# Kernel optimization log

Hardware: AMD Instinct MI355X
Metric: run time of the kernel (lower is better)

## Reference

```python
import jax, jax.numpy as jnp
import numpy as np

NEG_BIG = -1e30  # stand-in for -inf in the log-space eps state


def wkv_scan(w, u, k, v, alpha0, beta0, eps0):
    """Numerically-stable RWKV WKV recurrence.

    w: exp(time_decay) (D,), u: time_first (D,)
    k, v: (B, T, D); alpha0, beta0, eps0: (B, D)
    Returns wkv (B, T, D) and final state.
    """
    def step(carry, kv_t):
        alpha, beta, eps = carry
        kt, vt = kv_t  # (B, D)
        # output: (e^{u+k} v + alpha) / (e^{u+k} + beta), stabilized
        ww = u + kt
        tau = jnp.maximum(eps, ww)
        e1 = jnp.exp(eps - tau)
        e2 = jnp.exp(ww - tau)
        out = (e1 * alpha + e2 * vt) / (e1 * beta + e2)
        # state update with decay: alpha' = e^{-w} alpha + e^{k} v (log-space)
        ww2 = eps - w
        tau2 = jnp.maximum(ww2, kt)
        e1b = jnp.exp(ww2 - tau2)
        e2b = jnp.exp(kt - tau2)
        return (e1b * alpha + e2b * vt, e1b * beta + e2b, tau2), out

    kT = jnp.swapaxes(k, 0, 1)  # (T, B, D)
    vT = jnp.swapaxes(v, 0, 1)
    (_, _, _), outs = jax.lax.scan(step, (alpha0, beta0, eps0), (kT, vT))
    return jnp.swapaxes(outs, 0, 1)  # (B, T, D)


def setup_inputs() -> dict:
    key = jax.random.key(0)
    ks = jax.random.split(key, 10)
    B, T, D = 4, 2048, 2048
    scale = 1.0 / np.sqrt(D)
    x = jax.random.normal(ks[0], (B, T, D), dtype=jnp.float32)
    time_decay = jax.random.uniform(ks[1], (D,), minval=-1.0, maxval=1.0)
    time_first = 0.1 * jax.random.normal(ks[2], (D,))
    time_mix_k = jax.random.uniform(ks[3], (1, 1, D))
    time_mix_v = jax.random.uniform(ks[4], (1, 1, D))
    time_mix_r = jax.random.uniform(ks[5], (1, 1, D))
    Wk = scale * jax.random.normal(ks[6], (D, D))
    Wv = scale * jax.random.normal(ks[7], (D, D))
    Wr = scale * jax.random.normal(ks[8], (D, D))
    Wo = scale * jax.random.normal(ks[9], (D, D))
    return {"x": x, "time_decay": time_decay, "time_first": time_first,
            "time_mix_k": time_mix_k, "time_mix_v": time_mix_v,
            "time_mix_r": time_mix_r, "Wk": Wk, "Wv": Wv, "Wr": Wr, "Wo": Wo}


def reference(x, time_decay, time_first, time_mix_k, time_mix_v, time_mix_r,
              Wk, Wv, Wr, Wo):
    B, T, D = x.shape
    # time_shift: prepend zero init_x, drop last token
    last_x = jnp.concatenate([jnp.zeros((B, 1, D), x.dtype), x[:, :-1, :]], axis=1)
    k = jnp.einsum('btd,ed->bte', x * time_mix_k + last_x * (1 - time_mix_k), Wk)
    v = jnp.einsum('btd,ed->bte', x * time_mix_v + last_x * (1 - time_mix_v), Wv)
    r = jnp.einsum('btd,ed->bte', x * time_mix_r + last_x * (1 - time_mix_r), Wr)
    sr = jax.nn.sigmoid(r)
    w = jnp.exp(time_decay)
    alpha0 = jnp.zeros((B, D), x.dtype)
    beta0 = jnp.zeros((B, D), x.dtype)
    eps0 = jnp.full((B, D), NEG_BIG, x.dtype)
    wkv = wkv_scan(w, time_first, k, v, alpha0, beta0, eps0)
    return jnp.einsum('btd,ed->bte', wkv * sr, Wo)
```

## Files before the change

### kernel.cpp

```cpp
#include <hip/hip_runtime.h>
#include <stdint.h>

typedef __bf16 bf16x8 __attribute__((ext_vector_type(8)));
typedef float f32x4 __attribute__((ext_vector_type(4)));

#define BM 128
#define BN 128
#define BK 64

__global__ void cvt4_bf16(const float* __restrict__ w0, const float* __restrict__ w1,
                          const float* __restrict__ w2, const float* __restrict__ w3,
                          __bf16* __restrict__ o0, __bf16* __restrict__ o1,
                          __bf16* __restrict__ o2, __bf16* __restrict__ o3,
                          long DD) {
    long idx = ((long)blockIdx.x * blockDim.x + threadIdx.x) * 8;
    if (idx >= 4 * DD) return;
    int w = (int)(idx / DD);
    long off = idx - (long)w * DD;
    const float* in = (w == 0) ? w0 : (w == 1) ? w1 : (w == 2) ? w2 : w3;
    __bf16* out     = (w == 0) ? o0 : (w == 1) ? o1 : (w == 2) ? o2 : o3;
    f32x4 a = *(const f32x4*)(in + off);
    f32x4 b = *(const f32x4*)(in + off + 4);
    bf16x8 o;
#pragma unroll
    for (int i = 0; i < 4; ++i) { o[i] = (__bf16)a[i]; o[i + 4] = (__bf16)b[i]; }
    *(bf16x8*)(out + off) = o;
}

__global__ void mix3_kernel(const float* __restrict__ x,
                            const float* __restrict__ mk,
                            const float* __restrict__ mv,
                            const float* __restrict__ mr,
                            __bf16* __restrict__ ok, __bf16* __restrict__ ov,
                            __bf16* __restrict__ orr,
                            int T, int D, long total) {
    long idx = ((long)blockIdx.x * blockDim.x + threadIdx.x) * 8;
    if (idx >= total) return;
    int d = (int)(idx % D);
    long bt = idx / D;
    int t = (int)(bt % T);

    f32x4 x0 = *(const f32x4*)(x + idx);
    f32x4 x1 = *(const f32x4*)(x + idx + 4);
    f32x4 l0 = {}, l1 = {};
    if (t != 0) {
        l0 = *(const f32x4*)(x + idx - D);
        l1 = *(const f32x4*)(x + idx - D + 4);
    }
    const float* mw[3] = {mk, mv, mr};
    __bf16* ow[3] = {ok, ov, orr};
#pragma unroll
    for (int s = 0; s < 3; ++s) {
        f32x4 m0 = *(const f32x4*)(mw[s] + d);
        f32x4 m1 = *(const f32x4*)(mw[s] + d + 4);
        bf16x8 o;
#pragma unroll
        for (int i = 0; i < 4; ++i) {
            o[i]     = (__bf16)(x0[i] * m0[i] + l0[i] * (1.0f - m0[i]));
            o[i + 4] = (__bf16)(x1[i] * m1[i] + l1[i] * (1.0f - m1[i]));
        }
        *(bf16x8*)(ow[s] + idx) = o;
    }
}

template <typename CT>
__device__ __attribute__((always_inline))
void gemm_body(const __bf16* __restrict__ A, const __bf16* __restrict__ Bt,
               CT* __restrict__ C, int M, int N, int K) {
    __shared__ __align__(16) __bf16 sA[BM * BK];
    __shared__ __align__(16) __bf16 sB[BN * BK];

    const int tid  = threadIdx.x;
    const int lane = tid & 63;
    const int wave = tid >> 6;
    const int m0 = blockIdx.y * BM;
    const int n0 = blockIdx.x * BN;
    const int wm = (wave & 1) * 64;
    const int wn = (wave >> 1) * 64;

    const int l8 = lane >> 3;
    const int c8 = lane & 7;
    const int cg = c8 ^ l8;

    const int q  = lane >> 4;
    const int ml = lane & 15;

    f32x4 acc[4][4] = {};

    for (int k0 = 0; k0 < K; k0 += BK) {
#pragma unroll
        for (int i = 0; i < 4; ++i) {
            const int cl  = wave * 4 + i;
            const int row = cl * 8 + l8;
            const __bf16* gA = A  + (long)(m0 + row) * K + (k0 + cg * 8);
            const __bf16* gB = Bt + (long)(n0 + row) * K + (k0 + cg * 8);
            __builtin_amdgcn_global_load_lds(
                (const __attribute__((address_space(1))) void*)gA,
                (__attribute__((address_space(3))) void*)(sA + cl * 512), 16, 0, 0);
            __builtin_amdgcn_global_load_lds(
                (const __attribute__((address_space(1))) void*)gB,
                (__attribute__((address_space(3))) void*)(sB + cl * 512), 16, 0, 0);
        }
        __syncthreads();

#pragma unroll
        for (int kk = 0; kk < BK; kk += 32) {
            bf16x8 af[4], bfr[4];
#pragma unroll
            for (int i = 0; i < 4; ++i) {
                int row = wm + i * 16 + ml;
                int cl  = ((kk >> 3) + q) ^ (row & 7);
                af[i] = *(const bf16x8*)(sA + row * BK + cl * 8);
            }
#pragma unroll
            for (int j = 0; j < 4; ++j) {
                int row = wn + j * 16 + ml;
                int cl  = ((kk >> 3) + q) ^ (row & 7);
                bfr[j] = *(const bf16x8*)(sB + row * BK + cl * 8);
            }
#pragma unroll
            for (int i = 0; i < 4; ++i)
#pragma unroll
                for (int j = 0; j < 4; ++j)
                    acc[i][j] = __builtin_amdgcn_mfma_f32_16x16x32_bf16(
                        af[i], bfr[j], acc[i][j], 0, 0, 0);
        }
        __syncthreads();
    }

#pragma unroll
    for (int i = 0; i < 4; ++i)
#pragma unroll
        for (int j = 0; j < 4; ++j)
#pragma unroll
            for (int rg = 0; rg < 4; ++rg) {
                int row = m0 + wm + i * 16 + q * 4 + rg;
                int col = n0 + wn + j * 16 + ml;
                C[(long)row * N + col] = (CT)acc[i][j][rg];
            }
}

template <typename CT>
__global__ __launch_bounds__(256, 3)
void gemm_bt(const __bf16* __restrict__ A, const __bf16* __restrict__ Bt,
             CT* __restrict__ C, int M, int N, int K) {
    gemm_body<CT>(A, Bt, C, M, N, K);
}

__global__ __launch_bounds__(256, 3)
void gemm_bt2(const __bf16* __restrict__ A0, const __bf16* __restrict__ A1,
              const __bf16* __restrict__ B0, const __bf16* __restrict__ B1,
              __bf16* __restrict__ C0, __bf16* __restrict__ C1,
              int M, int N, int K) {
    if (blockIdx.z == 0) gemm_body<__bf16>(A0, B0, C0, M, N, K);
    else                 gemm_body<__bf16>(A1, B1, C1, M, N, K);
}

__global__ void wkv_pass1(const float* __restrict__ kk, const __bf16* __restrict__ vv,
                          const float* __restrict__ td,
                          float* __restrict__ al, float* __restrict__ bl,
                          float* __restrict__ el,
                          int Bn, int T, int D, int C, int L) {
    int gid = blockIdx.x * blockDim.x + threadIdx.x;
    int BD = Bn * D;
    if (gid >= BD * C) return;
    int c  = gid / BD;
    int bd = gid - c * BD;
    int b  = bd / D;
    int d  = bd - b * D;

    float w = __expf(td[d]);
    float alpha = 0.f, beta = 0.f, eps = -1e30f;
    long base = ((long)b * T + (long)c * L) * D + d;

    const int P = 8;
    float kb0[P], vb0[P], kb1[P], vb1[P];

    auto step = [&](float kt, float vt) {
        float ww2  = eps - w;
        float tau2 = fmaxf(ww2, kt);
        float e1b  = __expf(ww2 - tau2);
        float e2b  = __expf(kt - tau2);
        alpha = e1b * alpha + e2b * vt;
        beta  = e1b * beta + e2b;
        eps   = tau2;
    };

#pragma unroll
    for (int j = 0; j < P; ++j) {
        long o = base + (long)j * D;
        kb0[j] = kk[o]; vb0[j] = (float)vv[o];
    }
    for (int t0 = 0; t0 < L; t0 += 2 * P) {
#pragma unroll
        for (int j = 0; j < P; ++j) {
            long o = base + (long)(t0 + P + j) * D;
            kb1[j] = kk[o]; vb1[j] = (float)vv[o];
        }
#pragma unroll
        for (int j = 0; j < P; ++j) step(kb0[j], vb0[j]);
        if (t0 + 2 * P < L) {
#pragma unroll
            for (int j = 0; j < P; ++j) {
                long o = base + (long)(t0 + 2 * P + j) * D;
                kb0[j] = kk[o]; vb0[j] = (float)vv[o];
            }
        }
#pragma unroll
        for (int j = 0; j < P; ++j) step(kb1[j], vb1[j]);
    }
    al[gid] = alpha; bl[gid] = beta; el[gid] = eps;
}

__global__ void wkv_combine(const float* __restrict__ al, const float* __restrict__ bl,
                            const float* __restrict__ el, const float* __restrict__ td,
                            float* __restrict__ ai, float* __restrict__ bi,
                            float* __restrict__ ei,
                            int Bn, int D, int C, int L) {
    int bd = blockIdx.x * blockDim.x + threadIdx.x;
    int BD = Bn * D;
    if (bd >= BD) return;
    int d = bd % D;
    float wL = __expf(td[d]) * (float)L;
    float a = 0.f, b2 = 0.f, e = -1e30f;
    for (int c = 0; c < C; ++c) {
        int idx = c * BD + bd;
        ai[idx] = a; bi[idx] = b2; ei[idx] = e;
        float ed  = e - wL;
        float la = al[idx], lb = bl[idx], le = el[idx];
        float tau = fmaxf(ed, le);
        float e1  = __expf(ed - tau);
        float e2  = __expf(le - tau);
        a  = a * e1 + la * e2;
        b2 = b2 * e1 + lb * e2;
        e  = tau;
    }
}

__global__ void wkv_pass2(const float* __restrict__ kk, const __bf16* __restrict__ vv,
                          const __bf16* __restrict__ rr,
                          const float* __restrict__ td, const float* __restrict__ tf,
                          const float* __restrict__ ai, const float* __restrict__ bi,
                          const float* __restrict__ ei,
                          __bf16* __restrict__ out,
                          int Bn, int T, int D, int C, int L) {
    int gid = blockIdx.x * blockDim.x + threadIdx.x;
    int BD = Bn * D;
    if (gid >= BD * C) return;
    int c  = gid / BD;
    int bd = gid - c * BD;
    int b  = bd / D;
    int d  = bd - b * D;

    float u = tf[d];
    float w = __expf(td[d]);
    float alpha = ai[gid], beta = bi[gid], eps = ei[gid];
    long base = ((long)b * T + (long)c * L) * D + d;

    const int P = 8;
    float kb0[P], vb0[P], rb0[P], kb1[P], vb1[P], rb1[P];

    auto step = [&](float kt, float vt, float rt, int tIdx) {
        float ww  = u + kt;
        float tau = fmaxf(eps, ww);
        float e1  = __expf(eps - tau);
        float e2  = __expf(ww - tau);
        float num = e1 * alpha + e2 * vt;
        float den = e1 * beta + e2;
        float o_  = num * __builtin_amdgcn_rcpf(den);
        float ww2  = eps - w;
        float tau2 = fmaxf(ww2, kt);
        float e1b  = __expf(ww2 - tau2);
        float e2b  = __expf(kt - tau2);
        alpha = e1b * alpha + e2b * vt;
        beta  = e1b * beta + e2b;
        eps   = tau2;
        float sr = __builtin_amdgcn_rcpf(1.0f + __expf(-rt));
        out[base + (long)tIdx * D] = (__bf16)(o_ * sr);
    };

#pragma unroll
    for (int j = 0; j < P; ++j) {
        long o = base + (long)j * D;
        kb0[j] = kk[o]; vb0[j] = (float)vv[o]; rb0[j] = (float)rr[o];
    }
    for (int t0 = 0; t0 < L; t0 += 2 * P) {
#pragma unroll
        for (int j = 0; j < P; ++j) {
            long o = base + (long)(t0 + P + j) * D;
            kb1[j] = kk[o]; vb1[j] = (float)vv[o]; rb1[j] = (float)rr[o];
        }
#pragma unroll
        for (int j = 0; j < P; ++j) step(kb0[j], vb0[j], rb0[j], t0 + j);
        if (t0 + 2 * P < L) {
#pragma unroll
            for (int j = 0; j < P; ++j) {
                long o = base + (long)(t0 + 2 * P + j) * D;
                kb0[j] = kk[o]; vb0[j] = (float)vv[o]; rb0[j] = (float)rr[o];
            }
        }
#pragma unroll
        for (int j = 0; j < P; ++j) step(kb1[j], vb1[j], rb1[j], t0 + P + j);
    }
}

extern "C" void kernel_launch(void* const* d_in, const int* in_sizes, int n_in,
                              void* d_out, int out_size, void* d_ws, size_t ws_size,
                              hipStream_t stream) {
    const float* x  = (const float*)d_in[0];
    const float* td = (const float*)d_in[1];
    const float* tf = (const float*)d_in[2];
    const float* mk = (const float*)d_in[3];
    const float* mv = (const float*)d_in[4];
    const float* mr = (const float*)d_in[5];
    const float* Wk = (const float*)d_in[6];
    const float* Wv = (const float*)d_in[7];
    const float* Wr = (const float*)d_in[8];
    const float* Wo = (const float*)d_in[9];
    float* out = (float*)d_out;

    const int D = in_sizes[1];
    const int T = 2048;
    const long total = (long)in_sizes[0];
    const int Bn = (int)(total / ((long)T * D));
    const int M = Bn * T;
    const long DD = (long)D * D;
    const int C = 32;
    const int L = T / C;
    const int BD = Bn * D;
    const int S = BD * C;

    char* p = (char*)d_ws;
    __bf16* xmk = (__bf16*)p;            p += total * 2;
    __bf16* xmv = (__bf16*)p;            p += total * 2;
    __bf16* xmr = (__bf16*)p;            p += total * 2;
    __bf16* wkb = (__bf16*)p;            p += DD * 2;
    __bf16* wvb = (__bf16*)p;            p += DD * 2;
    __bf16* wrb = (__bf16*)p;            p += DD * 2;
    __bf16* wob = (__bf16*)p;            p += DD * 2;
    __bf16* vb  = (__bf16*)p;            p += total * 2;
    __bf16* rb  = (__bf16*)p;            p += total * 2;

    float*  kf = (float*)xmv;
    __bf16* xo = xmk;
    float*  st = (float*)wkb;
    float *al = st, *bl = st + S, *el = st + 2 * S;
    float *ai = st + 3 * S, *bi = st + 4 * S, *ei = st + 5 * S;

    dim3 mixGrid((unsigned)((total / 8 + 255) / 256));
    dim3 cvtGrid((unsigned)((4 * DD / 8 + 255) / 256));
    dim3 gemmGrid(D / BN, M / BM);
    dim3 gemm2Grid(D / BN, M / BM, 2);
    dim3 p12Grid((S + 255) / 256);
    dim3 cmbGrid((BD + 255) / 256);

    cvt4_bf16<<<cvtGrid, 256, 0, stream>>>(Wk, Wv, Wr, Wo, wkb, wvb, wrb, wob, DD);
    mix3_kernel<<<mixGrid, 256, 0, stream>>>(x, mk, mv, mr, xmk, xmv, xmr, T, D, total);

    gemm_bt2<<<gemm2Grid, 256, 0, stream>>>(xmv, xmr, wvb, wrb, vb, rb, M, D, D);
    gemm_bt<float><<<gemmGrid, 256, 0, stream>>>(xmk, wkb, kf, M, D, D);

    wkv_pass1<<<p12Grid, 256, 0, stream>>>(kf, vb, td, al, bl, el, Bn, T, D, C, L);
    wkv_combine<<<cmbGrid, 256, 0, stream>>>(al, bl, el, td, ai, bi, ei, Bn, D, C, L);
    wkv_pass2<<<p12Grid, 256, 0, stream>>>(kf, vb, rb, td, tf, ai, bi, ei, xo,
                                           Bn, T, D, C, L);

    gemm_bt<float><<<gemmGrid, 256, 0, stream>>>(xo, wob, out, M, D, D);
}
```

Measured before the change: 544.3 us.

## Merge weight-convert and mix kernels, fold chunk-combine scan into pass2

Fuses the bf16 weight conversion and the time-mix kernel into a single launch that splits work by block index. Removes the separate wkv_combine kernel: each pass2 thread now recomputes its chunk's prefix state by scanning the summaries of all earlier chunks itself. This drops two launches and the intermediate ai/bi/ei buffers, at the cost of redundant O(C) work per thread and load imbalance, since later chunks scan more prefixes.

```diff
diff --git a/kernel.cpp b/kernel.cpp
--- a/kernel.cpp
+++ b/kernel.cpp
@@ -8,58 +8,58 @@
 #define BN 128
 #define BK 64
 
-__global__ void cvt4_bf16(const float* __restrict__ w0, const float* __restrict__ w1,
-                          const float* __restrict__ w2, const float* __restrict__ w3,
-                          __bf16* __restrict__ o0, __bf16* __restrict__ o1,
-                          __bf16* __restrict__ o2, __bf16* __restrict__ o3,
-                          long DD) {
-    long idx = ((long)blockIdx.x * blockDim.x + threadIdx.x) * 8;
-    if (idx >= 4 * DD) return;
-    int w = (int)(idx / DD);
-    long off = idx - (long)w * DD;
-    const float* in = (w == 0) ? w0 : (w == 1) ? w1 : (w == 2) ? w2 : w3;
-    __bf16* out     = (w == 0) ? o0 : (w == 1) ? o1 : (w == 2) ? o2 : o3;
-    f32x4 a = *(const f32x4*)(in + off);
-    f32x4 b = *(const f32x4*)(in + off + 4);
-    bf16x8 o;
-#pragma unroll
-    for (int i = 0; i < 4; ++i) { o[i] = (__bf16)a[i]; o[i + 4] = (__bf16)b[i]; }
-    *(bf16x8*)(out + off) = o;
-}
-
-__global__ void mix3_kernel(const float* __restrict__ x,
-                            const float* __restrict__ mk,
-                            const float* __restrict__ mv,
+__global__ void prep_kernel(const float* __restrict__ w0, const float* __restrict__ w1,
+                            const float* __restrict__ w2, const float* __restrict__ w3,
+                            __bf16* __restrict__ o0, __bf16* __restrict__ o1,
+                            __bf16* __restrict__ o2, __bf16* __restrict__ o3,
+                            long DD, unsigned cvtBlocks,
+                            const float* __restrict__ x,
+                            const float* __restrict__ mk, const float* __restrict__ mv,
                             const float* __restrict__ mr,
                             __bf16* __restrict__ ok, __bf16* __restrict__ ov,
                             __bf16* __restrict__ orr,
                             int T, int D, long total) {
-    long idx = ((long)blockIdx.x * blockDim.x + threadIdx.x) * 8;
-    if (idx >= total) return;
-    int d = (int)(idx % D);
-    long bt = idx / D;
-    int t = (int)(bt % T);
-
-    f32x4 x0 = *(const f32x4*)(x + idx);
-    f32x4 x1 = *(const f32x4*)(x + idx + 4);
-    f32x4 l0 = {}, l1 = {};
-    if (t != 0) {
-        l0 = *(const f32x4*)(x + idx - D);
-        l1 = *(const f32x4*)(x + idx - D + 4);
-    }
-    const float* mw[3] = {mk, mv, mr};
-    __bf16* ow[3] = {ok, ov, orr};
-#pragma unroll
-    for (int s = 0; s < 3; ++s) {
-        f32x4 m0 = *(const f32x4*)(mw[s] + d);
-        f32x4 m1 = *(const f32x4*)(mw[s] + d + 4);
+    if (blockIdx.x < cvtBlocks) {
+        long idx = ((long)blockIdx.x * blockDim.x + threadIdx.x) * 8;
+        if (idx >= 4 * DD) return;
+        int w = (int)(idx / DD);
+        long off = idx - (long)w * DD;
+        const float* in = (w == 0) ? w0 : (w == 1) ? w1 : (w == 2) ? w2 : w3;
+        __bf16* out     = (w == 0) ? o0 : (w == 1) ? o1 : (w == 2) ? o2 : o3;
+        f32x4 a = *(const f32x4*)(in + off);
+        f32x4 b = *(const f32x4*)(in + off + 4);
         bf16x8 o;
 #pragma unroll
-        for (int i = 0; i < 4; ++i) {
-            o[i]     = (__bf16)(x0[i] * m0[i] + l0[i] * (1.0f - m0[i]));
-            o[i + 4] = (__bf16)(x1[i] * m1[i] + l1[i] * (1.0f - m1[i]));
-        }
-        *(bf16x8*)(ow[s] + idx) = o;
+        for (int i = 0; i < 4; ++i) { o[i] = (__bf16)a[i]; o[i + 4] = (__bf16)b[i]; }
+        *(bf16x8*)(out + off) = o;
+    } else {
+        long idx = ((long)(blockIdx.x - cvtBlocks) * blockDim.x + threadIdx.x) * 8;
+        if (idx >= total) return;
+        int d = (int)(idx % D);
+        long bt = idx / D;
+        int t = (int)(bt % T);
+
+        f32x4 x0 = *(const f32x4*)(x + idx);
+        f32x4 x1 = *(const f32x4*)(x + idx + 4);
+        f32x4 l0 = {}, l1 = {};
+        if (t != 0) {
+            l0 = *(const f32x4*)(x + idx - D);
+            l1 = *(const f32x4*)(x + idx - D + 4);
+        }
+        const float* mw[3] = {mk, mv, mr};
+        __bf16* ow[3] = {ok, ov, orr};
+#pragma unroll
+        for (int s = 0; s < 3; ++s) {
+            f32x4 m0 = *(const f32x4*)(mw[s] + d);
+            f32x4 m1 = *(const f32x4*)(mw[s] + d + 4);
+            bf16x8 o;
+#pragma unroll
+            for (int i = 0; i < 4; ++i) {
+                o[i]     = (__bf16)(x0[i] * m0[i] + l0[i] * (1.0f - m0[i]));
+                o[i + 4] = (__bf16)(x1[i] * m1[i] + l1[i] * (1.0f - m1[i]));
+            }
+            *(bf16x8*)(ow[s] + idx) = o;
+        }
     }
 }
 
@@ -212,36 +212,11 @@
     al[gid] = alpha; bl[gid] = beta; el[gid] = eps;
 }
 
-__global__ void wkv_combine(const float* __restrict__ al, const float* __restrict__ bl,
-                            const float* __restrict__ el, const float* __restrict__ td,
-                            float* __restrict__ ai, float* __restrict__ bi,
-                            float* __restrict__ ei,
-                            int Bn, int D, int C, int L) {
-    int bd = blockIdx.x * blockDim.x + threadIdx.x;
-    int BD = Bn * D;
-    if (bd >= BD) return;
-    int d = bd % D;
-    float wL = __expf(td[d]) * (float)L;
-    float a = 0.f, b2 = 0.f, e = -1e30f;
-    for (int c = 0; c < C; ++c) {
-        int idx = c * BD + bd;
-        ai[idx] = a; bi[idx] = b2; ei[idx] = e;
-        float ed  = e - wL;
-        float la = al[idx], lb = bl[idx], le = el[idx];
-        float tau = fmaxf(ed, le);
-        float e1  = __expf(ed - tau);
-        float e2  = __expf(le - tau);
-        a  = a * e1 + la * e2;
-        b2 = b2 * e1 + lb * e2;
-        e  = tau;
-    }
-}
-
 __global__ void wkv_pass2(const float* __restrict__ kk, const __bf16* __restrict__ vv,
                           const __bf16* __restrict__ rr,
                           const float* __restrict__ td, const float* __restrict__ tf,
-                          const float* __restrict__ ai, const float* __restrict__ bi,
-                          const float* __restrict__ ei,
+                          const float* __restrict__ al, const float* __restrict__ bl,
+                          const float* __restrict__ el,
                           __bf16* __restrict__ out,
                           int Bn, int T, int D, int C, int L) {
     int gid = blockIdx.x * blockDim.x + threadIdx.x;
@@ -254,7 +229,23 @@
 
     float u = tf[d];
     float w = __expf(td[d]);
-    float alpha = ai[gid], beta = bi[gid], eps = ei[gid];
+
+    float alpha = 0.f, beta = 0.f, eps = -1e30f;
+    {
+        float wL = w * (float)L;
+        for (int cc = 0; cc < c; ++cc) {
+            int idx = cc * BD + bd;
+            float ed  = eps - wL;
+            float la = al[idx], lb = bl[idx], le = el[idx];
+            float tau = fmaxf(ed, le);
+            float e1  = __expf(ed - tau);
+            float e2  = __expf(le - tau);
+            alpha = alpha * e1 + la * e2;
+            beta  = beta * e1 + lb * e2;
+            eps   = tau;
+        }
+    }
+
     long base = ((long)b * T + (long)c * L) * D + d;
 
     const int P = 8;
@@ -345,24 +336,24 @@
     __bf16* xo = xmk;
     float*  st = (float*)wkb;
     float *al = st, *bl = st + S, *el = st + 2 * S;
-    float *ai = st + 3 * S, *bi = st + 4 * S, *ei = st + 5 * S;
-
-    dim3 mixGrid((unsigned)((total / 8 + 255) / 256));
-    dim3 cvtGrid((unsigned)((4 * DD / 8 + 255) / 256));
+
+    unsigned cvtBlocks = (unsigned)((4 * DD / 8 + 255) / 256);
+    unsigned mixBlocks = (unsigned)((total / 8 + 255) / 256);
+    dim3 prepGrid(cvtBlocks + mixBlocks);
     dim3 gemmGrid(D / BN, M / BM);
     dim3 gemm2Grid(D / BN, M / BM, 2);
     dim3 p12Grid((S + 255) / 256);
-    dim3 cmbGrid((BD + 255) / 256);
-
-    cvt4_bf16<<<cvtGrid, 256, 0, stream>>>(Wk, Wv, Wr, Wo, wkb, wvb, wrb, wob, DD);
-    mix3_kernel<<<mixGrid, 256, 0, stream>>>(x, mk, mv, mr, xmk, xmv, xmr, T, D, total);
+
+    prep_kernel<<<prepGrid, 256, 0, stream>>>(Wk, Wv, Wr, Wo, wkb, wvb, wrb, wob,
+                                              DD, cvtBlocks,
+                                              x, mk, mv, mr, xmk, xmv, xmr,
+                                              T, D, total);
 
     gemm_bt2<<<gemm2Grid, 256, 0, stream>>>(xmv, xmr, wvb, wrb, vb, rb, M, D, D);
     gemm_bt<float><<<gemmGrid, 256, 0, stream>>>(xmk, wkb, kf, M, D, D);
 
     wkv_pass1<<<p12Grid, 256, 0, stream>>>(kf, vb, td, al, bl, el, Bn, T, D, C, L);
-    wkv_combine<<<cmbGrid, 256, 0, stream>>>(al, bl, el, td, ai, bi, ei, Bn, D, C, L);
-    wkv_pass2<<<p12Grid, 256, 0, stream>>>(kf, vb, rb, td, tf, ai, bi, ei, xo,
+    wkv_pass2<<<p12Grid, 256, 0, stream>>>(kf, vb, rb, td, tf, al, bl, el, xo,
                                            Bn, T, D, C, L);
 
     gemm_bt<float><<<gemmGrid, 256, 0, stream>>>(xo, wob, out, M, D, D);
```

After: 513.4 us. 1.06x faster.
